# Kernel optimization log

Hardware: AMD Instinct MI355X
Metric: run time of the kernel (lower is better)

## Reference

```python
import jax, jax.numpy as jnp
import numpy as np

B, C = 1, 1
D = H = W = 128          # volume depth/height/width (z, y, x)
V = U = 128              # detector rows (v) / cols (u)
A = 96                   # projection angles
N_STEPS = 128            # Joseph ray-marching steps
SX = SY = SD = 1.0       # voxel size (sd, sy, sx)
SU = SV = 1.0            # detector spacing (sv, su)


def setup_inputs() -> dict:
    key = jax.random.key(0)
    # model-facing volume [B, C, X, Y, Z]
    vol = jax.random.normal(key, (B, C, W, H, D), dtype=jnp.float32)
    angles = jnp.linspace(0.0, np.pi, A, endpoint=False).astype(jnp.float32)
    return {"vol": vol, "angles": angles}


def _corner(idx, size):
    """Floor/ceil corner indices + zero-padded linear weights (align_corners=True,
    padding_mode='zeros' semantics of F.grid_sample)."""
    i0f = jnp.floor(idx)
    frac = idx - i0f
    i0 = i0f.astype(jnp.int32)
    i1 = i0 + 1
    w0 = jnp.where((i0 >= 0) & (i0 < size), 1.0 - frac, 0.0)
    w1 = jnp.where((i1 >= 0) & (i1 < size), frac, 0.0)
    return jnp.clip(i0, 0, size - 1), jnp.clip(i1, 0, size - 1), w0, w1


def reference(vol, angles):
    # [B,C,X,Y,Z] -> [B,C,D,H,W] (z,y,x ordering used internally)
    v_zyx = jnp.transpose(vol, (0, 1, 4, 3, 2))
    cos_t = jnp.cos(angles)[:, None]   # [A,1]
    sin_t = jnp.sin(angles)[:, None]   # [A,1]
    u = (jnp.arange(U, dtype=jnp.float32) - (U - 1) / 2.0) * SU   # [U]
    v = (jnp.arange(V, dtype=jnp.float32) - (V - 1) / 2.0) * SV   # [V]
    # half ray length = half in-plane diagonal
    T = 0.5 * float(np.sqrt(((W - 1) * SX) ** 2 + ((H - 1) * SY) ** 2))
    delta_t = 2.0 * T / float(N_STEPS)

    x_base = -u[None, :] * sin_t   # [A,U] ray point at t=0
    y_base = u[None, :] * cos_t    # [A,U]
    # z depends only on detector row v; constant along the ray
    z_idx = v / SD + (D - 1) / 2.0                     # [V]
    z0, z1, wz0, wz1 = _corner(z_idx, D)
    z0, z1 = z0[:, None], z1[:, None]                  # [V,1]
    wz0, wz1 = wz0[:, None], wz1[:, None]

    t_vals = -T + (jnp.arange(N_STEPS, dtype=jnp.float32) + 0.5) * delta_t

    def step(acc, t):
        x_idx = (x_base + t * cos_t) / SX + (W - 1) / 2.0   # [A,U]
        y_idx = (y_base + t * sin_t) / SY + (H - 1) / 2.0   # [A,U]
        x0, x1, wx0, wx1 = [a[:, None, :] for a in _corner(x_idx, W)]  # [A,1,U]
        y0, y1, wy0, wy1 = [a[:, None, :] for a in _corner(y_idx, H)]  # [A,1,U]
        g = lambda zi, yi, xi: v_zyx[:, :, zi, yi, xi]      # -> [B,C,A,V,U]
        s = (wz0 * (wy0 * (wx0 * g(z0, y0, x0) + wx1 * g(z0, y0, x1))
                    + wy1 * (wx0 * g(z0, y1, x0) + wx1 * g(z0, y1, x1)))
             + wz1 * (wy0 * (wx0 * g(z1, y0, x0) + wx1 * g(z1, y0, x1))
                      + wy1 * (wx0 * g(z1, y1, x0) + wx1 * g(z1, y1, x1))))
        return acc + s, None

    acc0 = jnp.zeros((B, C, A, V, U), dtype=vol.dtype)
    acc, _ = jax.lax.scan(jax.checkpoint(step), acc0, t_vals)
    sino = acc * jnp.float32(delta_t)            # [B,C,A,V,U]
    # model-facing sinogram [B,C,X=U,A,Z=V]
    return jnp.transpose(sino, (0, 1, 4, 2, 3))
```

## Files before the change

### kernel.cpp

```cpp
#include <hip/hip_runtime.h>
#include <hip/hip_fp16.h>

namespace {
constexpr int A_N = 96;
constexpr int U_N = 128;
constexpr int V_N = 128;
constexpr int W_N = 128;
constexpr int H_N = 128;
constexpr int NSTEPS = 128;
constexpr float T_HALF = 89.80256121069154f;
constexpr float DT = 1.4031650189170554f;
constexpr float INV_DT = 1.0f / DT;
constexpr int PAD = 6;
constexpr int WP = W_N + 2 * PAD;
constexpr int ROW_BYTES = WP * 256;
constexpr int ZT = 8;
constexpr int RAYS_PER_WAVE = 8;
constexpr int WAVES_PER_BLOCK = 4;
constexpr int RAYS_PER_BLOCK = RAYS_PER_WAVE * WAVES_PER_BLOCK;
constexpr int BLOCK_THREADS = 256;
constexpr size_t VOLP_COLS = (size_t)WP * WP;
constexpr size_t VOLP_BYTES = VOLP_COLS * 256;
constexpr size_t SINO = (size_t)U_N * A_N * V_N;
}

typedef __attribute__((ext_vector_type(4))) unsigned int u32x4;

__device__ __forceinline__ unsigned int packh2(float a, float b) {
    return (unsigned int)__half_as_ushort(__float2half_rn(a)) |
           ((unsigned int)__half_as_ushort(__float2half_rn(b)) << 16);
}

__global__ __launch_bounds__(256) void vol_pad_f16(
    const float* __restrict__ vol, unsigned int* __restrict__ volp)
{
    const int idx = blockIdx.x * 256 + threadIdx.x;
    if (idx >= (int)(VOLP_COLS * 16)) return;
    const int zo  = idx & 15;
    const int col = idx >> 4;
    const int yp = col % WP;
    const int xp = col / WP;
    const int x = xp - PAD;
    const int y = yp - PAD;
    uint4 o = make_uint4(0u, 0u, 0u, 0u);
    if ((unsigned)x < 128u && (unsigned)y < 128u) {
        const float* src = vol + (((size_t)x * 128 + y) << 7) + zo * 8;
        const float4 f0 = *(const float4*)(src);
        const float4 f1 = *(const float4*)(src + 4);
        o.x = packh2(f0.x, f0.y);
        o.y = packh2(f0.z, f0.w);
        o.z = packh2(f1.x, f1.y);
        o.w = packh2(f1.z, f1.w);
    }
    *(uint4*)((char*)volp + (size_t)col * 256 + zo * 16) = o;
}

#define ISSUE4(p, q0, q1, q2, q3)                                        \
    asm volatile("global_load_dwordx4 %0, %4, off\n\t"                   \
                 "global_load_dwordx4 %1, %4, off offset:128\n\t"        \
                 "global_load_dwordx4 %2, %4, off offset:256\n\t"        \
                 "global_load_dwordx4 %3, %4, off offset:384"            \
                 : "=&v"(q0), "=&v"(q1), "=&v"(q2), "=&v"(q3)            \
                 : "v"(p))

#define WAIT_VM8()  do { asm volatile("s_waitcnt vmcnt(8)" ::: "memory"); \
                         __builtin_amdgcn_sched_barrier(0); } while (0)
#define WAIT_VM0()  do { asm volatile("s_waitcnt vmcnt(0)" ::: "memory"); \
                         __builtin_amdgcn_sched_barrier(0); } while (0)

__global__ __launch_bounds__(BLOCK_THREADS, 4) void joseph_fwd_inc(
    const unsigned short* __restrict__ volp,
    const float* __restrict__ angles,
    float* __restrict__ dst, float scale)
{
    const int zo = threadIdx.x & (ZT - 1);
    const int r  = (threadIdx.x >> 3) & 7;
    const int wv = threadIdx.x >> 6;
    const int bx = (int)blockIdx.x;
    const int xt = (bx == 0) ? 1 : (bx == 1) ? 2 : (bx == 2) ? 0 : 3;
    const int u_i = xt * RAYS_PER_BLOCK + wv * RAYS_PER_WAVE + r;
    const int a   = blockIdx.y;

    const int spseg = NSTEPS / gridDim.z;
    const int i0 = blockIdx.z * spseg;
    const int i1 = i0 + spseg;

    const float ang = angles[a];
    const float cv = cosf(ang);
    const float sv = sinf(ang);
    const float up = (float)u_i - 63.5f;
    const float xb = fmaf(-up, sv, 63.5f);
    const float yb = fmaf( up, cv, 63.5f);

    float tlo = -2.f * T_HALF, thi = 2.f * T_HALF;
    if (fabsf(cv) > 1e-6f) {
        const float ta = (-1.f - xb) / cv, tb = (128.f - xb) / cv;
        tlo = fmaxf(tlo, fminf(ta, tb));
        thi = fminf(thi, fmaxf(ta, tb));
    } else if (xb <= -1.f || xb >= 128.f) { thi = tlo - 1.f; }
    if (fabsf(sv) > 1e-6f) {
        const float ta = (-1.f - yb) / sv, tb = (128.f - yb) / sv;
        tlo = fmaxf(tlo, fminf(ta, tb));
        thi = fminf(thi, fmaxf(ta, tb));
    } else if (yb <= -1.f || yb >= 128.f) { thi = tlo - 1.f; }
    const int ilo = (int)floorf(fmaf(tlo + T_HALF, INV_DT, -0.5f)) - 1;
    const int ihi = (int)ceilf (fmaf(thi + T_HALF, INV_DT, -0.5f)) + 1;
    int lo = min(max(ilo, i0), i1);
    int hi = min(max(ihi + 1, i0), i1);
    lo &= ~1;
    hi = (hi + 1) & ~1;

    const char* __restrict__ volc = (const char*)volp;
    const int laneb = zo << 4;

    __half2 hacc[8];
    float accf[16];
#pragma unroll
    for (int j = 0; j < 8; ++j) hacc[j] = __float2half2_rn(0.f);
#pragma unroll
    for (int k = 0; k < 16; ++k) accf[k] = 0.f;

    auto base_of = [&](float i_f, float& fx, float& fy) -> const char* {
        const float tf = fmaf(i_f + 0.5f, DT, -T_HALF);
        const float xi = fmaf(tf, cv, xb);
        const float yi = fmaf(tf, sv, yb);
        const float fx0 = floorf(xi);
        const float fy0 = floorf(yi);
        fx = xi - fx0;
        fy = yi - fy0;
        const int x0 = (int)fx0;
        const int y0 = (int)fy0;
        return volc + ((((x0 + PAD) * WP + (y0 + PAD)) << 8) + laneb);
    };

    auto cons = [&](u32x4 q00l, u32x4 q00h, u32x4 q01l, u32x4 q01h,
                    u32x4 q10l, u32x4 q10h, u32x4 q11l, u32x4 q11h,
                    float fx, float fy) {
        const float wx0 = 1.f - fx;
        const float wy0 = 1.f - fy;
        const __half2 w00 = __float2half2_rn(wx0 * wy0);
        const __half2 w01 = __float2half2_rn(wx0 * fy);
        const __half2 w10 = __float2half2_rn(fx  * wy0);
        const __half2 w11 = __float2half2_rn(fx  * fy);
#pragma unroll
        for (int j = 0; j < 4; ++j) {
            hacc[j] = __hfma2(w00, __builtin_bit_cast(__half2, (unsigned int)q00l[j]), hacc[j]);
            hacc[j] = __hfma2(w01, __builtin_bit_cast(__half2, (unsigned int)q01l[j]), hacc[j]);
            hacc[j] = __hfma2(w10, __builtin_bit_cast(__half2, (unsigned int)q10l[j]), hacc[j]);
            hacc[j] = __hfma2(w11, __builtin_bit_cast(__half2, (unsigned int)q11l[j]), hacc[j]);
            hacc[4 + j] = __hfma2(w00, __builtin_bit_cast(__half2, (unsigned int)q00h[j]), hacc[4 + j]);
            hacc[4 + j] = __hfma2(w01, __builtin_bit_cast(__half2, (unsigned int)q01h[j]), hacc[4 + j]);
            hacc[4 + j] = __hfma2(w10, __builtin_bit_cast(__half2, (unsigned int)q10h[j]), hacc[4 + j]);
            hacc[4 + j] = __hfma2(w11, __builtin_bit_cast(__half2, (unsigned int)q11h[j]), hacc[4 + j]);
        }
    };

    auto flush = [&]() {
#pragma unroll
        for (int j = 0; j < 8; ++j) {
            const float2 f = __half22float2(hacc[j]);
            accf[2 * j]     += f.x;
            accf[2 * j + 1] += f.y;
            hacc[j] = __float2half2_rn(0.f);
        }
    };

    if (lo < hi) {
        u32x4 A0, A1, A2, A3, A4, A5, A6, A7;
        u32x4 B0, B1, B2, B3, B4, B5, B6, B7;
        float fxA, fyA, fxB, fyB;
        int kc = 0;
        int i = lo;
        {
            const char* p  = base_of((float)i, fxA, fyA);
            const char* p2 = p + ROW_BYTES;
            ISSUE4(p,  A0, A1, A2, A3);
            ISSUE4(p2, A4, A5, A6, A7);
        }
        for (;;) {
            {
                const char* p  = base_of((float)(i + 1), fxB, fyB);
                const char* p2 = p + ROW_BYTES;
                ISSUE4(p,  B0, B1, B2, B3);
                ISSUE4(p2, B4, B5, B6, B7);
            }
            WAIT_VM8();
            cons(A0, A1, A2, A3, A4, A5, A6, A7, fxA, fyA);
            i += 2;
            if (i >= hi) {
                WAIT_VM0();
                cons(B0, B1, B2, B3, B4, B5, B6, B7, fxB, fyB);
                break;
            }
            {
                const char* p  = base_of((float)i, fxA, fyA);
                const char* p2 = p + ROW_BYTES;
                ISSUE4(p,  A0, A1, A2, A3);
                ISSUE4(p2, A4, A5, A6, A7);
            }
            WAIT_VM8();
            cons(B0, B1, B2, B3, B4, B5, B6, B7, fxB, fyB);
            if (((++kc) & 1) == 0) flush();
        }
    }
    flush();

    float* op = dst + (size_t)blockIdx.z * SINO + ((size_t)u_i * A_N + a) * V_N;
    float* opl = op + 8 * zo;
    float* oph = op + 64 + 8 * zo;
    *(float4*)(opl)     = make_float4(accf[0]  * scale, accf[1]  * scale, accf[2]  * scale, accf[3]  * scale);
    *(float4*)(opl + 4) = make_float4(accf[4]  * scale, accf[5]  * scale, accf[6]  * scale, accf[7]  * scale);
    *(float4*)(oph)     = make_float4(accf[8]  * scale, accf[9]  * scale, accf[10] * scale, accf[11] * scale);
    *(float4*)(oph + 4) = make_float4(accf[12] * scale, accf[13] * scale, accf[14] * scale, accf[15] * scale);
}

__global__ __launch_bounds__(256) void reduce_segs(
    const float4* __restrict__ p, float4* __restrict__ out, int nseg)
{
    const size_t i = (size_t)blockIdx.x * 256 + threadIdx.x;
    const size_t q = SINO / 4;
    float4 s = p[i];
    for (int k = 1; k < nseg; ++k) {
        const float4 b = p[i + (size_t)k * q];
        s.x += b.x; s.y += b.y; s.z += b.z; s.w += b.w;
    }
    out[i] = make_float4(s.x * DT, s.y * DT, s.z * DT, s.w * DT);
}

__global__ __launch_bounds__(256) void joseph_fwd_f32(
    const float* __restrict__ vol,
    const float* __restrict__ angles,
    float* __restrict__ out)
{
    const int zo  = threadIdx.x & 15;
    const int r   = threadIdx.x >> 4;
    const int u_i = blockIdx.x * 16 + r;
    const int a   = blockIdx.y;

    const float ang = angles[a];
    const float c = cosf(ang);
    const float s = sinf(ang);
    const float u = (float)u_i - 63.5f;
    const float xb = fmaf(-u, s, 63.5f);
    const float yb = fmaf( u, c, 63.5f);

    const float* volz = vol + 8 * zo;
    float4 accA = make_float4(0.f, 0.f, 0.f, 0.f);
    float4 accB = make_float4(0.f, 0.f, 0.f, 0.f);

    for (int i = 0; i < NSTEPS; ++i) {
        const float t  = fmaf((float)i + 0.5f, DT, -T_HALF);
        const float xi = fmaf(t, c, xb);
        const float yi = fmaf(t, s, yb);
        const float fx0f = floorf(xi);
        const float fy0f = floorf(yi);
        const int x0 = (int)fx0f;
        const int y0 = (int)fy0f;
        const float fx = xi - fx0f;
        const float fy = yi - fy0f;
        const int x1 = x0 + 1;
        const int y1 = y0 + 1;
        const float wx0 = (x0 >= 0 && x0 < W_N) ? (1.f - fx) : 0.f;
        const float wx1 = (x1 >= 0 && x1 < W_N) ? fx : 0.f;
        const float wy0 = (y0 >= 0 && y0 < H_N) ? (1.f - fy) : 0.f;
        const float wy1 = (y1 >= 0 && y1 < H_N) ? fy : 0.f;
        if ((wx0 + wx1) == 0.f || (wy0 + wy1) == 0.f) continue;
        const int cx0 = min(max(x0, 0), W_N - 1);
        const int cx1 = min(max(x1, 0), W_N - 1);
        const int cy0 = min(max(y0, 0), H_N - 1);
        const int cy1 = min(max(y1, 0), H_N - 1);
        const float* p00 = volz + ((cx0 * H_N + cy0) << 7);
        const float* p01 = volz + ((cx1 * H_N + cy0) << 7);
        const float* p10 = volz + ((cx0 * H_N + cy1) << 7);
        const float* p11 = volz + ((cx1 * H_N + cy1) << 7);
        const float4 v00a = *(const float4*)(p00);
        const float4 v00b = *(const float4*)(p00 + 4);
        const float4 v01a = *(const float4*)(p01);
        const float4 v01b = *(const float4*)(p01 + 4);
        const float4 v10a = *(const float4*)(p10);
        const float4 v10b = *(const float4*)(p10 + 4);
        const float4 v11a = *(const float4*)(p11);
        const float4 v11b = *(const float4*)(p11 + 4);
        const float w00 = wx0 * wy0, w01 = wx1 * wy0, w10 = wx0 * wy1, w11 = wx1 * wy1;
        accA.x = fmaf(w00, v00a.x, fmaf(w01, v01a.x, fmaf(w10, v10a.x, fmaf(w11, v11a.x, accA.x))));
        accA.y = fmaf(w00, v00a.y, fmaf(w01, v01a.y, fmaf(w10, v10a.y, fmaf(w11, v11a.y, accA.y))));
        accA.z = fmaf(w00, v00a.z, fmaf(w01, v01a.z, fmaf(w10, v10a.z, fmaf(w11, v11a.z, accA.z))));
        accA.w = fmaf(w00, v00a.w, fmaf(w01, v01a.w, fmaf(w10, v10a.w, fmaf(w11, v11a.w, accA.w))));
        accB.x = fmaf(w00, v00b.x, fmaf(w01, v01b.x, fmaf(w10, v10b.x, fmaf(w11, v11b.x, accB.x))));
        accB.y = fmaf(w00, v00b.y, fmaf(w01, v01b.y, fmaf(w10, v10b.y, fmaf(w11, v11b.y, accB.y))));
        accB.z = fmaf(w00, v00b.z, fmaf(w01, v01b.z, fmaf(w10, v10b.z, fmaf(w11, v11b.z, accB.z))));
        accB.w = fmaf(w00, v00b.w, fmaf(w01, v01b.w, fmaf(w10, v10b.w, fmaf(w11, v11b.w, accB.w))));
    }

    float* op = out + ((size_t)u_i * A_N + a) * V_N + 8 * zo;
    *(float4*)(op)     = make_float4(accA.x * DT, accA.y * DT, accA.z * DT, accA.w * DT);
    *(float4*)(op + 4) = make_float4(accB.x * DT, accB.y * DT, accB.z * DT, accB.w * DT);
}

extern "C" void kernel_launch(void* const* d_in, const int* in_sizes, int n_in,
                              void* d_out, int out_size, void* d_ws, size_t ws_size,
                              hipStream_t stream) {
    const float* vol    = (const float*)d_in[0];
    const float* angles = (const float*)d_in[1];
    float* out          = (float*)d_out;

    const int pad_blocks = (int)((VOLP_COLS * 16 + 255) / 256);

    if (ws_size >= VOLP_BYTES) {
        unsigned int* volp = (unsigned int*)d_ws;
        hipLaunchKernelGGL(vol_pad_f16, dim3(pad_blocks), dim3(256), 0, stream, vol, volp);

        int nseg = 0;
        if (ws_size >= VOLP_BYTES + 4 * SINO * sizeof(float))      nseg = 4;
        else if (ws_size >= VOLP_BYTES + 2 * SINO * sizeof(float)) nseg = 2;

        if (nseg) {
            float* partial = (float*)((char*)d_ws + VOLP_BYTES);
            dim3 grid(U_N / RAYS_PER_BLOCK, A_N, nseg);
            hipLaunchKernelGGL(joseph_fwd_inc, grid, dim3(BLOCK_THREADS), 0, stream,
                               (const unsigned short*)volp, angles, partial, 1.0f);
            hipLaunchKernelGGL(reduce_segs, dim3(SINO / 4 / 256), dim3(256), 0, stream,
                               (const float4*)partial, (float4*)out, nseg);
        } else {
            dim3 grid(U_N / RAYS_PER_BLOCK, A_N, 1);
            hipLaunchKernelGGL(joseph_fwd_inc, grid, dim3(BLOCK_THREADS), 0, stream,
                               (const unsigned short*)volp, angles, out, DT);
        }
    } else {
        dim3 grid(U_N / 16, A_N);
        hipLaunchKernelGGL(joseph_fwd_f32, grid, dim3(256), 0, stream, vol, angles, out);
    }
}
```

Measured before the change: 116.6 us.

## Split ray steps across waves in a block and reduce in shared memory

Replaces the multi-segment launch, which wrote partial sinograms to workspace and summed them in a separate reduce kernel, with one fused kernel. Each block now covers 16 rays, and two wave pairs each march half of the steps. The two halves are combined through shared memory and scaled before the single global write. Block indices are also swizzled to spread angles and ray tiles across the grid. This removes a launch and the partial-buffer traffic, but uses only 2-way step splitting instead of up to 4-way and adds a block barrier.

```diff
diff --git a/kernel.cpp b/kernel.cpp
--- a/kernel.cpp
+++ b/kernel.cpp
@@ -16,8 +16,7 @@
 constexpr int ROW_BYTES = WP * 256;
 constexpr int ZT = 8;
 constexpr int RAYS_PER_WAVE = 8;
-constexpr int WAVES_PER_BLOCK = 4;
-constexpr int RAYS_PER_BLOCK = RAYS_PER_WAVE * WAVES_PER_BLOCK;
+constexpr int RAYS_PER_BLOCK = 16;
 constexpr int BLOCK_THREADS = 256;
 constexpr size_t VOLP_COLS = (size_t)WP * WP;
 constexpr size_t VOLP_BYTES = VOLP_COLS * 256;
@@ -68,22 +67,26 @@
 #define WAIT_VM0()  do { asm volatile("s_waitcnt vmcnt(0)" ::: "memory"); \
                          __builtin_amdgcn_sched_barrier(0); } while (0)
 
-__global__ __launch_bounds__(BLOCK_THREADS, 4) void joseph_fwd_inc(
+__global__ __launch_bounds__(BLOCK_THREADS, 4) void joseph_fwd_fused(
     const unsigned short* __restrict__ volp,
     const float* __restrict__ angles,
-    float* __restrict__ dst, float scale)
+    float* __restrict__ out)
 {
     const int zo = threadIdx.x & (ZT - 1);
-    const int r  = (threadIdx.x >> 3) & 7;
+    const int rw = (threadIdx.x >> 3) & 7;
     const int wv = threadIdx.x >> 6;
-    const int bx = (int)blockIdx.x;
-    const int xt = (bx == 0) ? 1 : (bx == 1) ? 2 : (bx == 2) ? 0 : 3;
-    const int u_i = xt * RAYS_PER_BLOCK + wv * RAYS_PER_WAVE + r;
-    const int a   = blockIdx.y;
-
-    const int spseg = NSTEPS / gridDim.z;
-    const int i0 = blockIdx.z * spseg;
-    const int i1 = i0 + spseg;
+    const int ray = (wv & 1) * 8 + rw;
+    const int shalf = wv >> 1;
+
+    const int lin = (int)blockIdx.x + 8 * (int)blockIdx.y;
+    const int swz = (lin & 7) * 96 + (lin >> 3);
+    const int a   = swz >> 3;
+    const int xtr = swz & 7;
+    const int xt = (xtr & 1) ? (4 + (xtr >> 1)) : (3 - (xtr >> 1));
+    const int u_i = xt * RAYS_PER_BLOCK + ray;
+
+    const int i0 = shalf * (NSTEPS / 2);
+    const int i1 = i0 + NSTEPS / 2;
 
     const float ang = angles[a];
     const float cv = cosf(ang);
@@ -205,26 +208,35 @@
     }
     flush();
 
-    float* op = dst + (size_t)blockIdx.z * SINO + ((size_t)u_i * A_N + a) * V_N;
-    float* opl = op + 8 * zo;
-    float* oph = op + 64 + 8 * zo;
-    *(float4*)(opl)     = make_float4(accf[0]  * scale, accf[1]  * scale, accf[2]  * scale, accf[3]  * scale);
-    *(float4*)(opl + 4) = make_float4(accf[4]  * scale, accf[5]  * scale, accf[6]  * scale, accf[7]  * scale);
-    *(float4*)(oph)     = make_float4(accf[8]  * scale, accf[9]  * scale, accf[10] * scale, accf[11] * scale);
-    *(float4*)(oph + 4) = make_float4(accf[12] * scale, accf[13] * scale, accf[14] * scale, accf[15] * scale);
-}
-
-__global__ __launch_bounds__(256) void reduce_segs(
-    const float4* __restrict__ p, float4* __restrict__ out, int nseg)
-{
-    const size_t i = (size_t)blockIdx.x * 256 + threadIdx.x;
-    const size_t q = SINO / 4;
-    float4 s = p[i];
-    for (int k = 1; k < nseg; ++k) {
-        const float4 b = p[i + (size_t)k * q];
-        s.x += b.x; s.y += b.y; s.z += b.z; s.w += b.w;
-    }
-    out[i] = make_float4(s.x * DT, s.y * DT, s.z * DT, s.w * DT);
+    __shared__ float part[RAYS_PER_BLOCK][V_N];
+    if (shalf == 1) {
+        float* p0 = &part[ray][8 * zo];
+        float* p1 = &part[ray][64 + 8 * zo];
+        *(float4*)(p0)     = make_float4(accf[0],  accf[1],  accf[2],  accf[3]);
+        *(float4*)(p0 + 4) = make_float4(accf[4],  accf[5],  accf[6],  accf[7]);
+        *(float4*)(p1)     = make_float4(accf[8],  accf[9],  accf[10], accf[11]);
+        *(float4*)(p1 + 4) = make_float4(accf[12], accf[13], accf[14], accf[15]);
+    }
+    __syncthreads();
+    if (shalf == 0) {
+        const float* p0 = &part[ray][8 * zo];
+        const float* p1 = &part[ray][64 + 8 * zo];
+        const float4 q0 = *(const float4*)(p0);
+        const float4 q1 = *(const float4*)(p0 + 4);
+        const float4 q2 = *(const float4*)(p1);
+        const float4 q3 = *(const float4*)(p1 + 4);
+        float* op = out + ((size_t)u_i * A_N + a) * V_N;
+        float* opl = op + 8 * zo;
+        float* oph = op + 64 + 8 * zo;
+        *(float4*)(opl)     = make_float4((accf[0]  + q0.x) * DT, (accf[1]  + q0.y) * DT,
+                                          (accf[2]  + q0.z) * DT, (accf[3]  + q0.w) * DT);
+        *(float4*)(opl + 4) = make_float4((accf[4]  + q1.x) * DT, (accf[5]  + q1.y) * DT,
+                                          (accf[6]  + q1.z) * DT, (accf[7]  + q1.w) * DT);
+        *(float4*)(oph)     = make_float4((accf[8]  + q2.x) * DT, (accf[9]  + q2.y) * DT,
+                                          (accf[10] + q2.z) * DT, (accf[11] + q2.w) * DT);
+        *(float4*)(oph + 4) = make_float4((accf[12] + q3.x) * DT, (accf[13] + q3.y) * DT,
+                                          (accf[14] + q3.z) * DT, (accf[15] + q3.w) * DT);
+    }
 }
 
 __global__ __launch_bounds__(256) void joseph_fwd_f32(
@@ -309,23 +321,9 @@
     if (ws_size >= VOLP_BYTES) {
         unsigned int* volp = (unsigned int*)d_ws;
         hipLaunchKernelGGL(vol_pad_f16, dim3(pad_blocks), dim3(256), 0, stream, vol, volp);
-
-        int nseg = 0;
-        if (ws_size >= VOLP_BYTES + 4 * SINO * sizeof(float))      nseg = 4;
-        else if (ws_size >= VOLP_BYTES + 2 * SINO * sizeof(float)) nseg = 2;
-
-        if (nseg) {
-            float* partial = (float*)((char*)d_ws + VOLP_BYTES);
-            dim3 grid(U_N / RAYS_PER_BLOCK, A_N, nseg);
-            hipLaunchKernelGGL(joseph_fwd_inc, grid, dim3(BLOCK_THREADS), 0, stream,
-                               (const unsigned short*)volp, angles, partial, 1.0f);
-            hipLaunchKernelGGL(reduce_segs, dim3(SINO / 4 / 256), dim3(256), 0, stream,
-                               (const float4*)partial, (float4*)out, nseg);
-        } else {
-            dim3 grid(U_N / RAYS_PER_BLOCK, A_N, 1);
-            hipLaunchKernelGGL(joseph_fwd_inc, grid, dim3(BLOCK_THREADS), 0, stream,
-                               (const unsigned short*)volp, angles, out, DT);
-        }
+        dim3 grid(U_N / RAYS_PER_BLOCK, A_N);
+        hipLaunchKernelGGL(joseph_fwd_fused, grid, dim3(BLOCK_THREADS), 0, stream,
+                           (const unsigned short*)volp, angles, out);
     } else {
         dim3 grid(U_N / 16, A_N);
         hipLaunchKernelGGL(joseph_fwd_f32, grid, dim3(256), 0, stream, vol, angles, out);
```

New measurement: 105.9 us (median of 2 runs). 9.2% less time.
